# Kernel tuning notes

Hardware: AMD Instinct MI355X
Metric: run time of the kernel (lower is better)

The kernel has to match this reference:

```python
import jax, jax.numpy as jnp
import numpy as np


def setup_inputs() -> dict:
    key = jax.random.key(0)
    k1, k2, k3 = jax.random.split(key, 3)
    B, N, F, U = 8, 2048, 128, 128
    A = jax.random.uniform(k1, (B, N, N), dtype=jnp.float32)   # dense nonneg adjacency
    X = jax.random.normal(k2, (B, N, F), dtype=jnp.float32)
    W = jax.random.normal(k3, (F, U), dtype=jnp.float32)
    bias = jnp.zeros((U,), dtype=jnp.float32)
    p = jnp.zeros((1,), dtype=jnp.float32)
    q = jnp.zeros((1,), dtype=jnp.float32)
    return {"A": A, "X": X, "W": W, "bias": bias, "p": p, "q": q}


def reference(A, X, W, bias, p, q):
    # learn_pqr path of MyGCN: A_ = D @ (A + q*I) @ D with D = diag(k^-0.25),
    # k = p + (1-p)*colsum(A). Diag matmuls expressed as broadcasted scaling (same math).
    B, N, _ = A.shape
    ps = jax.nn.sigmoid(p)          # shape (1,)
    qs = jax.nn.sigmoid(q)
    Dr = jnp.sum(A, axis=1)          # [B, N]  (K.sum axis=1)
    k_vec = ps + (1.0 - ps) * Dr     # [B, N]
    k_inv_root = jnp.sqrt(k_vec) ** -0.5   # k^{-0.25}
    k_clean = jnp.where(jnp.isinf(k_inv_root), 0.0, k_inv_root)  # [B, N]
    I = jnp.eye(N, dtype=A.dtype)
    AqI = A + qs[0] * I              # [B, N, N]
    A_ = k_clean[:, :, None] * AqI * k_clean[:, None, :]
    XW = jnp.einsum('bnf,fu->bnu', X, W)        # [B, N, U]
    A_XW = jnp.einsum('bnm,bmu->bnu', A_, XW)   # [B, N, U]
    out = A_XW + bias
    return jax.nn.relu(out)
```

## Files before the change

kernel.cpp:

```cpp
#include <hip/hip_runtime.h>
#include <stdint.h>

#define N 2048
#define F 128
#define UDIM 128

typedef __attribute__((ext_vector_type(8))) __bf16 bf16x8;
typedef __attribute__((ext_vector_type(8))) unsigned short us8;
typedef __attribute__((ext_vector_type(4))) float f32x4;

__device__ __forceinline__ unsigned short f2bf(float f) {
  union { float f; uint32_t u; } v; v.f = f;
  uint32_t u = v.u;
  return (unsigned short)((u + 0x7FFFu + ((u >> 16) & 1u)) >> 16);
}
__device__ __forceinline__ float bf2f(unsigned short u) {
  union { uint32_t u; float f; } v; v.u = ((uint32_t)u) << 16; return v.f;
}
__device__ __forceinline__ uint32_t cvtpk(float lo, float hi) {
  uint32_t r;
  asm("v_cvt_pk_bf16_f32 %0, %1, %2" : "=v"(r) : "v"(lo), "v"(hi));
  return r;
}
__device__ __forceinline__ void async_load16(const void* g, void* l) {
  typedef const __attribute__((address_space(1))) uint32_t* gp_t;
  typedef __attribute__((address_space(3))) uint32_t* lp_t;
  __builtin_amdgcn_global_load_lds((gp_t)(uintptr_t)g, (lp_t)(uint32_t)(uintptr_t)l, 16, 0, 0);
}

__global__ __launch_bounds__(256, 4)
void gcn_pass1(const float* __restrict__ A, const float* __restrict__ X,
               const float* __restrict__ W, float* __restrict__ partial,
               unsigned short* __restrict__ Z) {
  __shared__ __align__(16) unsigned short Wl[128 * 128];
  __shared__ __align__(16) unsigned short Xl[32 * 128];

  const int bid = blockIdx.x;
  const int t = threadIdx.x;

  if (bid < 1024) {
    const int b = bid >> 7;
    const int rc = (bid >> 1) & 63;
    const int j = (bid & 1) * 1024 + t * 4;
    const float* ap = A + (size_t)b * N * N + (size_t)rc * 32 * N + j;
    float s0 = 0.f, s1 = 0.f, s2 = 0.f, s3 = 0.f;
    #pragma unroll 4
    for (int rr = 0; rr < 32; ++rr) {
      float4 v = *(const float4*)(ap + (size_t)rr * N);
      s0 += v.x; s1 += v.y; s2 += v.z; s3 += v.w;
    }
    float4 s; s.x = s0; s.y = s1; s.z = s2; s.w = s3;
    *(float4*)&partial[((size_t)b * 64 + rc) * N + j] = s;
    return;
  }

  const int zid = bid - 1024;
  const int lane = t & 63;
  const int wid = t >> 6;
  const int b = zid >> 6;
  const int i0 = (zid & 63) << 5;

  {
    const int u = t & 127;
    const int khalf = t >> 7;
    #pragma unroll
    for (int g = 0; g < 8; ++g) {
      const int k0 = khalf * 64 + g * 8;
      float v[8];
      #pragma unroll
      for (int e = 0; e < 8; ++e) v[e] = W[(size_t)(k0 + e) * 128 + u];
      uint4 w;
      w.x = cvtpk(v[0], v[1]); w.y = cvtpk(v[2], v[3]);
      w.z = cvtpk(v[4], v[5]); w.w = cvtpk(v[6], v[7]);
      const int slot = khalf * 8 + g;
      *(uint4*)&Wl[u * 128 + ((slot ^ (u & 7)) * 8)] = w;
    }
  }
  {
    const int r = t >> 3;
    const float* xp = X + ((size_t)b * N + i0 + r) * F + (t & 7) * 8;
    #pragma unroll
    for (int h = 0; h < 2; ++h) {
      float4 v0 = *(const float4*)(xp + h * 64);
      float4 v1 = *(const float4*)(xp + h * 64 + 4);
      uint4 w;
      w.x = cvtpk(v0.x, v0.y); w.y = cvtpk(v0.z, v0.w);
      w.z = cvtpk(v1.x, v1.y); w.w = cvtpk(v1.z, v1.w);
      const int slot = (t & 7) + h * 8;
      *(uint4*)&Xl[r * 128 + ((slot ^ (r & 7)) * 8)] = w;
    }
  }
  __syncthreads();

  f32x4 acc[2][2];
  #pragma unroll
  for (int a = 0; a < 2; ++a)
    #pragma unroll
    for (int c = 0; c < 2; ++c) { f32x4 z = {0.f, 0.f, 0.f, 0.f}; acc[a][c] = z; }

  const int u0 = wid * 32;
  #pragma unroll
  for (int kc = 0; kc < 4; ++kc) {
    bf16x8 af[2], bfv[2];
    #pragma unroll
    for (int ut = 0; ut < 2; ++ut) {
      const int u = u0 + ut * 16 + (lane & 15);
      const int sl = ((kc * 4 + (lane >> 4)) ^ (u & 7)) * 8;
      af[ut] = *(const bf16x8*)&Wl[u * 128 + sl];
    }
    #pragma unroll
    for (int it = 0; it < 2; ++it) {
      const int rr = it * 16 + (lane & 15);
      const int sl = ((kc * 4 + (lane >> 4)) ^ (rr & 7)) * 8;
      bfv[it] = *(const bf16x8*)&Xl[rr * 128 + sl];
    }
    #pragma unroll
    for (int ut = 0; ut < 2; ++ut)
      #pragma unroll
      for (int it = 0; it < 2; ++it)
        acc[ut][it] = __builtin_amdgcn_mfma_f32_16x16x32_bf16(af[ut], bfv[it], acc[ut][it], 0, 0, 0);
  }

  #pragma unroll
  for (int ut = 0; ut < 2; ++ut)
    #pragma unroll
    for (int it = 0; it < 2; ++it) {
      const int ic = i0 + it * 16 + (lane & 15);
      #pragma unroll
      for (int rg = 0; rg < 4; ++rg) {
        const int u = u0 + ut * 16 + (lane >> 4) * 4 + rg;
        Z[((size_t)b * UDIM + u) * N + ic] = f2bf(acc[ut][it][rg]);
      }
    }
}

__global__ __launch_bounds__(256, 4)
void gcn_kcl(const float* __restrict__ partial, const float* __restrict__ pptr,
             float* __restrict__ kcl) {
  const int t = threadIdx.x;
  const int b = blockIdx.x >> 3;
  const int jj = (blockIdx.x & 7) * 256 + t;
  float s = 0.f;
  #pragma unroll 8
  for (int rc = 0; rc < 64; ++rc)
    s += partial[((size_t)b * 64 + rc) * N + jj];
  const float sp = 1.0f / (1.0f + __expf(-pptr[0]));
  const float k = sp + (1.0f - sp) * s;
  float rv = rsqrtf(sqrtf(k));
  if (isinf(rv)) rv = 0.f;
  kcl[b * N + jj] = rv;
}

__global__ __launch_bounds__(256, 2)
void gcn_gemm(const float* __restrict__ A, const unsigned short* __restrict__ Z,
              const float* __restrict__ kcl, const float* __restrict__ bias,
              const float* __restrict__ qptr, float* __restrict__ out) {
  __shared__ __align__(16) unsigned short Abuf[3 * 32 * 64];
  __shared__ __align__(16) unsigned short Ybuf[3 * 128 * 64];
  __shared__ __align__(16) float kcs[2048];

  const int t = threadIdx.x;
  const int lane = t & 63;
  const int wid = t >> 6;
  const int wr = wid >> 1;
  const int wc = wid & 1;

  const int bid = blockIdx.x;
  const int b = bid & 7;
  const int i0 = (bid >> 3) << 5;

  const float qs = 1.0f / (1.0f + __expf(-qptr[0]));

  const int r = t >> 3;
  const int c8 = t & 7;
  const float* Ap = A + (size_t)b * N * N + (size_t)(i0 + r) * N + c8 * 8;
  const unsigned short* Zb = Z + (size_t)b * UDIM * N;

  const int a_woff = r * 64 + ((c8 ^ (r & 7)) * 8);
  const int y_u = t >> 3;
  const int y_wavebase = (t & ~63) * 8;

  {
    float4 v0 = *(const float4*)&kcl[b * N + t * 8];
    float4 v1 = *(const float4*)&kcl[b * N + t * 8 + 4];
    *(float4*)&kcs[t * 8] = v0;
    *(float4*)&kcs[t * 8 + 4] = v1;
  }
  __syncthreads();

  f32x4 acc[4];
  #pragma unroll
  for (int i = 0; i < 4; ++i) { f32x4 z = {0.f, 0.f, 0.f, 0.f}; acc[i] = z; }

  float4 a0A, a1A, a0B, a1B;

  auto issueY = [&](int kt, int buf) {
    const int k0 = kt * 64;
    #pragma unroll
    for (int rnd = 0; rnd < 4; ++rnd) {
      const int u = rnd * 32 + y_u;
      const int c16 = (t & 7) ^ (u & 7);
      async_load16(Zb + (size_t)u * N + k0 + c16 * 8, &Ybuf[buf * 8192 + rnd * 2048 + y_wavebase]);
    }
  };
  auto compute = [&](int cur) {
    const unsigned short* Ac = Abuf + cur * 2048;
    const unsigned short* Yc = Ybuf + cur * 8192;
    #pragma unroll
    for (int kk = 0; kk < 2; ++kk) {
      const int ar = 16 * wr + (lane & 15);
      const int as = ((kk * 4 + (lane >> 4)) ^ (ar & 7)) * 8;
      bf16x8 af = *(const bf16x8*)&Ac[ar * 64 + as];
      #pragma unroll
      for (int ut = 0; ut < 4; ++ut) {
        const int u = 64 * wc + ut * 16 + (lane & 15);
        const int bs = ((kk * 4 + (lane >> 4)) ^ (u & 7)) * 8;
        bf16x8 bfv = *(const bf16x8*)&Yc[u * 64 + bs];
        acc[ut] = __builtin_amdgcn_mfma_f32_16x16x32_bf16(af, bfv, acc[ut], 0, 0, 0);
      }
    }
  };

#define SB __builtin_amdgcn_sched_barrier(0)
#define ISSUE_A(KT, R0, R1) { R0 = *(const float4*)(Ap + (KT) * 64); R1 = *(const float4*)(Ap + (KT) * 64 + 4); }
#define CVT_A(BUF, R0, R1, K0) { \
    float4 kj0 = *(const float4*)&kcs[(K0) + c8 * 8]; \
    float4 kj1 = *(const float4*)&kcs[(K0) + c8 * 8 + 4]; \
    uint4 w; \
    w.x = cvtpk(R0.x * kj0.x, R0.y * kj0.y); \
    w.y = cvtpk(R0.z * kj0.z, R0.w * kj0.w); \
    w.z = cvtpk(R1.x * kj1.x, R1.y * kj1.y); \
    w.w = cvtpk(R1.z * kj1.z, R1.w * kj1.w); \
    *(uint4*)&Abuf[(BUF) * 2048 + a_woff] = w; }

  asm volatile("s_waitcnt vmcnt(0) lgkmcnt(0)" ::: "memory");

  ISSUE_A(0, a0A, a1A); SB;
  ISSUE_A(1, a0B, a1B); SB;
  issueY(0, 0); SB;
  asm volatile("s_waitcnt vmcnt(6)" ::: "memory");
  CVT_A(0, a0A, a1A, 0); SB;
  ISSUE_A(2, a0A, a1A); SB;
  issueY(1, 1); SB;

#define GSTEP(KT, VM, R0, R1, DO_A, DO_Y)                          \
  {                                                                \
    asm volatile("s_waitcnt vmcnt(" #VM ")" ::: "memory");         \
    CVT_A(((KT) + 1) % 3, R0, R1, ((KT) + 1) * 64);                \
    asm volatile("s_waitcnt lgkmcnt(0)" ::: "memory");             \
    __builtin_amdgcn_s_barrier(); SB;                              \
    if (DO_A) { ISSUE_A((KT) + 3, R0, R1); } SB;                   \
    if (DO_Y) { issueY((KT) + 2, ((KT) + 2) % 3); } SB;            \
    __builtin_amdgcn_s_setprio(1);                                 \
    compute((KT) % 3);                                             \
    __builtin_amdgcn_s_setprio(0); SB;                             \
  }

  #pragma unroll 1
  for (int kt = 0; kt < 28; kt += 2) {
    GSTEP(kt,     6, a0B, a1B, true, true);
    GSTEP(kt + 1, 6, a0A, a1A, true, true);
  }
  GSTEP(28, 6, a0B, a1B, true, true);
  GSTEP(29, 6, a0A, a1A, false, true);
  asm volatile("s_waitcnt vmcnt(4)" ::: "memory");
  CVT_A(1, a0B, a1B, 31 * 64);
  asm volatile("s_waitcnt lgkmcnt(0)" ::: "memory");
  __builtin_amdgcn_s_barrier(); SB;
  compute(0);
  asm volatile("s_waitcnt vmcnt(0)" ::: "memory");
  __builtin_amdgcn_s_barrier(); SB;
  compute(1);
#undef GSTEP
#undef CVT_A
#undef ISSUE_A
#undef SB

  const int irow = i0 + 16 * wr + (lane >> 4) * 4;
  #pragma unroll
  for (int ut = 0; ut < 4; ++ut) {
    const int u = 64 * wc + ut * 16 + (lane & 15);
    const float bv = bias[u];
    #pragma unroll
    for (int rg = 0; rg < 4; ++rg) {
      const int i = irow + rg;
      const float zv = bf2f(Zb[(size_t)u * N + i]);
      const float kv = kcs[i];
      float vv = kv * acc[ut][rg] + qs * kv * kv * zv + bv;
      out[((size_t)b * N + i) * UDIM + u] = vv > 0.f ? vv : 0.f;
    }
  }
}

extern "C" void kernel_launch(void* const* d_in, const int* in_sizes, int n_in,
                              void* d_out, int out_size, void* d_ws, size_t ws_size,
                              hipStream_t stream) {
  (void)in_sizes; (void)n_in; (void)out_size; (void)ws_size;
  const float* A    = (const float*)d_in[0];
  const float* X    = (const float*)d_in[1];
  const float* W    = (const float*)d_in[2];
  const float* bias = (const float*)d_in[3];
  const float* p    = (const float*)d_in[4];
  const float* q    = (const float*)d_in[5];
  float* out = (float*)d_out;

  char* ws = (char*)d_ws;
  float* partial      = (float*)ws;
  float* kcl          = (float*)(ws + 4194304);
  unsigned short* Zb  = (unsigned short*)(ws + 4259840);

  gcn_pass1<<<dim3(1536), dim3(256), 0, stream>>>(A, X, W, partial, Zb);
  gcn_kcl<<<dim3(64), dim3(256), 0, stream>>>(partial, p, kcl);
  gcn_gemm<<<dim3(512), dim3(256), 0, stream>>>(A, Zb, kcl, bias, q, out);
}
```

Before: 57.34 us.

## Enlarge GEMM tile to 64 rows with 512-thread blocks and 2x2 wave fragments

The main GEMM kernel now uses 512-thread blocks, each covering 64 output rows instead of 32. The grid halves to 256 blocks and each wave computes a 2x2 grid of MFMA fragments. Each Z tile loaded into LDS is therefore shared by twice as many A rows, which cuts Z traffic and per-block overhead, and the wait counts are adjusted for the fewer Y loads per thread. The costs are a bigger LDS footprint, fewer blocks (256 blocks on a 256-CU part, one wave of work), and possibly lower occupancy.

```diff
diff --git a/kernel.cpp b/kernel.cpp
--- a/kernel.cpp
+++ b/kernel.cpp
@@ -151,23 +151,23 @@
   kcl[b * N + jj] = rv;
 }
 
-__global__ __launch_bounds__(256, 2)
+__global__ __launch_bounds__(512, 2)
 void gcn_gemm(const float* __restrict__ A, const unsigned short* __restrict__ Z,
               const float* __restrict__ kcl, const float* __restrict__ bias,
               const float* __restrict__ qptr, float* __restrict__ out) {
-  __shared__ __align__(16) unsigned short Abuf[3 * 32 * 64];
+  __shared__ __align__(16) unsigned short Abuf[3 * 64 * 64];
   __shared__ __align__(16) unsigned short Ybuf[3 * 128 * 64];
   __shared__ __align__(16) float kcs[2048];
 
   const int t = threadIdx.x;
   const int lane = t & 63;
   const int wid = t >> 6;
-  const int wr = wid >> 1;
-  const int wc = wid & 1;
+  const int wr = wid >> 2;
+  const int wc = wid & 3;
 
   const int bid = blockIdx.x;
   const int b = bid & 7;
-  const int i0 = (bid >> 3) << 5;
+  const int i0 = (bid >> 3) << 6;
 
   const float qs = 1.0f / (1.0f + __expf(-qptr[0]));
 
@@ -181,43 +181,51 @@
   const int y_wavebase = (t & ~63) * 8;
 
   {
-    float4 v0 = *(const float4*)&kcl[b * N + t * 8];
-    float4 v1 = *(const float4*)&kcl[b * N + t * 8 + 4];
-    *(float4*)&kcs[t * 8] = v0;
-    *(float4*)&kcs[t * 8 + 4] = v1;
+    float4 v0 = *(const float4*)&kcl[b * N + t * 4];
+    *(float4*)&kcs[t * 4] = v0;
   }
   __syncthreads();
 
-  f32x4 acc[4];
-  #pragma unroll
-  for (int i = 0; i < 4; ++i) { f32x4 z = {0.f, 0.f, 0.f, 0.f}; acc[i] = z; }
+  f32x4 acc[2][2];
+  #pragma unroll
+  for (int mf = 0; mf < 2; ++mf)
+    #pragma unroll
+    for (int uf = 0; uf < 2; ++uf) { f32x4 z = {0.f, 0.f, 0.f, 0.f}; acc[mf][uf] = z; }
 
   float4 a0A, a1A, a0B, a1B;
 
   auto issueY = [&](int kt, int buf) {
     const int k0 = kt * 64;
     #pragma unroll
-    for (int rnd = 0; rnd < 4; ++rnd) {
-      const int u = rnd * 32 + y_u;
+    for (int rnd = 0; rnd < 2; ++rnd) {
+      const int u = rnd * 64 + y_u;
       const int c16 = (t & 7) ^ (u & 7);
-      async_load16(Zb + (size_t)u * N + k0 + c16 * 8, &Ybuf[buf * 8192 + rnd * 2048 + y_wavebase]);
+      async_load16(Zb + (size_t)u * N + k0 + c16 * 8, &Ybuf[buf * 8192 + rnd * 4096 + y_wavebase]);
     }
   };
   auto compute = [&](int cur) {
-    const unsigned short* Ac = Abuf + cur * 2048;
+    const unsigned short* Ac = Abuf + cur * 4096;
     const unsigned short* Yc = Ybuf + cur * 8192;
     #pragma unroll
     for (int kk = 0; kk < 2; ++kk) {
-      const int ar = 16 * wr + (lane & 15);
-      const int as = ((kk * 4 + (lane >> 4)) ^ (ar & 7)) * 8;
-      bf16x8 af = *(const bf16x8*)&Ac[ar * 64 + as];
-      #pragma unroll
-      for (int ut = 0; ut < 4; ++ut) {
-        const int u = 64 * wc + ut * 16 + (lane & 15);
+      bf16x8 af[2], bfv[2];
+      #pragma unroll
+      for (int mf = 0; mf < 2; ++mf) {
+        const int ar = 32 * wr + mf * 16 + (lane & 15);
+        const int as = ((kk * 4 + (lane >> 4)) ^ (ar & 7)) * 8;
+        af[mf] = *(const bf16x8*)&Ac[ar * 64 + as];
+      }
+      #pragma unroll
+      for (int uf = 0; uf < 2; ++uf) {
+        const int u = 32 * wc + uf * 16 + (lane & 15);
         const int bs = ((kk * 4 + (lane >> 4)) ^ (u & 7)) * 8;
-        bf16x8 bfv = *(const bf16x8*)&Yc[u * 64 + bs];
-        acc[ut] = __builtin_amdgcn_mfma_f32_16x16x32_bf16(af, bfv, acc[ut], 0, 0, 0);
+        bfv[uf] = *(const bf16x8*)&Yc[u * 64 + bs];
       }
+      #pragma unroll
+      for (int mf = 0; mf < 2; ++mf)
+        #pragma unroll
+        for (int uf = 0; uf < 2; ++uf)
+          acc[mf][uf] = __builtin_amdgcn_mfma_f32_16x16x32_bf16(af[mf], bfv[uf], acc[mf][uf], 0, 0, 0);
     }
   };
 
@@ -231,14 +239,14 @@
     w.y = cvtpk(R0.z * kj0.z, R0.w * kj0.w); \
     w.z = cvtpk(R1.x * kj1.x, R1.y * kj1.y); \
     w.w = cvtpk(R1.z * kj1.z, R1.w * kj1.w); \
-    *(uint4*)&Abuf[(BUF) * 2048 + a_woff] = w; }
+    *(uint4*)&Abuf[(BUF) * 4096 + a_woff] = w; }
 
   asm volatile("s_waitcnt vmcnt(0) lgkmcnt(0)" ::: "memory");
 
   ISSUE_A(0, a0A, a1A); SB;
   ISSUE_A(1, a0B, a1B); SB;
   issueY(0, 0); SB;
-  asm volatile("s_waitcnt vmcnt(6)" ::: "memory");
+  asm volatile("s_waitcnt vmcnt(4)" ::: "memory");
   CVT_A(0, a0A, a1A, 0); SB;
   ISSUE_A(2, a0A, a1A); SB;
   issueY(1, 1); SB;
@@ -258,12 +266,12 @@
 
   #pragma unroll 1
   for (int kt = 0; kt < 28; kt += 2) {
-    GSTEP(kt,     6, a0B, a1B, true, true);
-    GSTEP(kt + 1, 6, a0A, a1A, true, true);
-  }
-  GSTEP(28, 6, a0B, a1B, true, true);
-  GSTEP(29, 6, a0A, a1A, false, true);
-  asm volatile("s_waitcnt vmcnt(4)" ::: "memory");
+    GSTEP(kt,     4, a0B, a1B, true, true);
+    GSTEP(kt + 1, 4, a0A, a1A, true, true);
+  }
+  GSTEP(28, 4, a0B, a1B, true, true);
+  GSTEP(29, 4, a0A, a1A, false, true);
+  asm volatile("s_waitcnt vmcnt(2)" ::: "memory");
   CVT_A(1, a0B, a1B, 31 * 64);
   asm volatile("s_waitcnt lgkmcnt(0)" ::: "memory");
   __builtin_amdgcn_s_barrier(); SB;
@@ -276,18 +284,21 @@
 #undef ISSUE_A
 #undef SB
 
-  const int irow = i0 + 16 * wr + (lane >> 4) * 4;
-  #pragma unroll
-  for (int ut = 0; ut < 4; ++ut) {
-    const int u = 64 * wc + ut * 16 + (lane & 15);
-    const float bv = bias[u];
-    #pragma unroll
-    for (int rg = 0; rg < 4; ++rg) {
-      const int i = irow + rg;
-      const float zv = bf2f(Zb[(size_t)u * N + i]);
-      const float kv = kcs[i];
-      float vv = kv * acc[ut][rg] + qs * kv * kv * zv + bv;
-      out[((size_t)b * N + i) * UDIM + u] = vv > 0.f ? vv : 0.f;
+  #pragma unroll
+  for (int mf = 0; mf < 2; ++mf) {
+    const int irow = i0 + 32 * wr + mf * 16 + (lane >> 4) * 4;
+    #pragma unroll
+    for (int uf = 0; uf < 2; ++uf) {
+      const int u = 32 * wc + uf * 16 + (lane & 15);
+      const float bv = bias[u];
+      #pragma unroll
+      for (int rg = 0; rg < 4; ++rg) {
+        const int i = irow + rg;
+        const float zv = bf2f(Zb[(size_t)u * N + i]);
+        const float kv = kcs[i];
+        float vv = kv * acc[mf][uf][rg] + qs * kv * kv * zv + bv;
+        out[((size_t)b * N + i) * UDIM + u] = vv > 0.f ? vv : 0.f;
+      }
     }
   }
 }
@@ -311,5 +322,5 @@
 
   gcn_pass1<<<dim3(1536), dim3(256), 0, stream>>>(A, X, W, partial, Zb);
   gcn_kcl<<<dim3(64), dim3(256), 0, stream>>>(partial, p, kcl);
-  gcn_gemm<<<dim3(512), dim3(256), 0, stream>>>(A, Zb, kcl, bias, q, out);
-}
+  gcn_gemm<<<dim3(256), dim3(512), 0, stream>>>(A, Zb, kcl, bias, q, out);
+}
```

Result: slower. 59.51 us (+3.8%).
